# Kernel tuning notes

Hardware: AMD Instinct MI355X
Metric: run time of the kernel (lower is better)

The kernel has to match this reference:

```python
import jax, jax.numpy as jnp
import numpy as np

D_MODEL = 1024
NUM_HEADS = 16
HEAD_DIM = D_MODEL // NUM_HEADS


def setup_inputs() -> dict:
    key = jax.random.key(0)
    ks = jax.random.split(key, 9)
    B, S = 2, 2048
    scale = 1.0 / np.sqrt(D_MODEL)
    inp = {
        "x": jax.random.normal(ks[0], (B, S, D_MODEL), dtype=jnp.float32),
        "Wq": jax.random.normal(ks[1], (D_MODEL, D_MODEL), dtype=jnp.float32) * scale,
        "bq": jnp.zeros((D_MODEL,), dtype=jnp.float32),
        "Wk": jax.random.normal(ks[2], (D_MODEL, D_MODEL), dtype=jnp.float32) * scale,
        "bk": jnp.zeros((D_MODEL,), dtype=jnp.float32),
        "Wv": jax.random.normal(ks[3], (D_MODEL, D_MODEL), dtype=jnp.float32) * scale,
        "bv": jnp.zeros((D_MODEL,), dtype=jnp.float32),
        "Wo": jax.random.normal(ks[4], (D_MODEL, D_MODEL), dtype=jnp.float32) * scale,
        "bo": jnpp_zeros(D_MODEL) if False else jnp.zeros((D_MODEL,), dtype=jnp.float32),
    }
    return inp


def reference(x, Wq, bq, Wk, bk, Wv, bv, Wo, bo):
    B, S, _ = x.shape
    # projections (torch Linear: y = x @ W.T + b; here W stored as [in, out])
    q = x @ Wq + bq  # [B,S,D]
    k = x @ Wk + bk
    v = x @ Wv + bv
    # split heads -> [B,H,S,hd]
    def split(t):
        return t.reshape(B, S, NUM_HEADS, HEAD_DIM).transpose(0, 2, 1, 3)
    q, k, v = split(q), split(k), split(v)
    scale = 1.0 / jnp.sqrt(jnp.asarray(HEAD_DIM, dtype=x.dtype))
    scores = jnp.einsum("bhqd,bhkd->bhqk", q, k) * scale  # [B,H,S,S]
    probs = jax.nn.softmax(scores, axis=-1)
    out = jnp.einsum("bhqk,bhkd->bhqd", probs, v)  # [B,H,S,hd]
    out = out.transpose(0, 2, 1, 3).reshape(B, S, D_MODEL)
    return out @ Wo + bo  # dropout is identity in eval mode
```

## Files before the change

### kernel.cpp

```cpp
#include <hip/hip_runtime.h>

#define D_MODEL 1024
#define NHEADS  16
#define HDIM    64
#define BATCH   2
#define SEQ     2048
#define M_TOK   (BATCH * SEQ)

typedef unsigned short u16;
typedef unsigned int   u32;
typedef __attribute__((ext_vector_type(8))) short  short8;
typedef __attribute__((ext_vector_type(4))) float  floatx4;
typedef __attribute__((ext_vector_type(2))) u32    u32x2;

#define GLOBAL_AS __attribute__((address_space(1)))
#define LDS_AS    __attribute__((address_space(3)))

static __device__ __forceinline__ void gload_lds16(const u16* g, u16* l) {
    __builtin_amdgcn_global_load_lds((const GLOBAL_AS u32*)g, (LDS_AS u32*)l, 16, 0, 0);
}

static __device__ __forceinline__ u16 f2bf(float f) {
    union { float f; u32 i; } v; v.f = f;
    u32 x = v.i;
    return (u16)((x + 0x7fffu + ((x >> 16) & 1u)) >> 16);
}

static __device__ __forceinline__ u32 cvtpk(float a, float b) {
    u32 r;
    asm("v_cvt_pk_bf16_f32 %0, %1, %2" : "=v"(r) : "v"(a), "v"(b));
    return r;
}

static __device__ __forceinline__ short8 ld8_cvt(const float* __restrict__ p) {
    float4 f0 = *(const float4*)(p);
    float4 f1 = *(const float4*)(p + 4);
    short8 r;
    r[0] = (short)f2bf(f0.x); r[1] = (short)f2bf(f0.y);
    r[2] = (short)f2bf(f0.z); r[3] = (short)f2bf(f0.w);
    r[4] = (short)f2bf(f1.x); r[5] = (short)f2bf(f1.y);
    r[6] = (short)f2bf(f1.z); r[7] = (short)f2bf(f1.w);
    return r;
}

__global__ __launch_bounds__(256) void zerofill_k(float* __restrict__ out, int n) {
    int i = blockIdx.x * 256 + threadIdx.x;
    if (i < n) out[i] = 0.f;
}

__global__ __launch_bounds__(256) void prep_k(const float* __restrict__ x,
                                              const float* __restrict__ W0,
                                              const float* __restrict__ W1,
                                              const float* __restrict__ W2,
                                              const float* __restrict__ W3,
                                              u16* __restrict__ WtBase,
                                              u16* __restrict__ Xb) {
    int z = blockIdx.z;
    int t = threadIdx.x;
    if (z == 4) {
        int blk = blockIdx.y * 32 + blockIdx.x;
        size_t i0 = ((size_t)blk * 256 + t) * 16;
        short8 v0 = ld8_cvt(x + i0);
        short8 v1 = ld8_cvt(x + i0 + 8);
        *(short8*)(Xb + i0)     = v0;
        *(short8*)(Xb + i0 + 8) = v1;
        return;
    }
    const float* W = (z == 0) ? W0 : (z == 1) ? W1 : (z == 2) ? W2 : W3;
    u16* Wt = WtBase + (size_t)z * 1024 * 1024;
    __shared__ u16 T[32][34];
    int bx = blockIdx.x * 32, by = blockIdx.y * 32;
    {
        int r = t >> 3, c4 = t & 7;
        float4 f = *(const float4*)(W + (size_t)(by + r) * 1024 + bx + c4 * 4);
        u32 lo = (u32)f2bf(f.x) | ((u32)f2bf(f.y) << 16);
        u32 hi = (u32)f2bf(f.z) | ((u32)f2bf(f.w) << 16);
        *(u32*)(&T[r][c4 * 4])     = lo;
        *(u32*)(&T[r][c4 * 4 + 2]) = hi;
    }
    __syncthreads();
    if (t < 128) {
        int n = t >> 2, seg = t & 3;
        short8 v;
#pragma unroll
        for (int i = 0; i < 8; ++i) v[i] = (short)T[seg * 8 + i][n];
        *(short8*)(Wt + (size_t)(bx + n) * 1024 + by + seg * 8) = v;
    }
}

template <int MODE, int OUTF32, int MI, int BK>
static __device__ __forceinline__ void gemm_core(u16* __restrict__ smem,
                                                 const u16* __restrict__ A,
                                                 const u16* __restrict__ Bt,
                                                 const float* __restrict__ bias,
                                                 float scale,
                                                 void* __restrict__ C,
                                                 int m0, int n0) {
    constexpr int RG   = BK / 8;
    constexpr int BUFG = (MI * 32 + 128) * RG;
    int tid  = threadIdx.x;
    int wave = tid >> 6, lane = tid & 63;
    int quad = lane >> 4, l15 = lane & 15;
    int wm = (wave & 1) * (MI * 16);
    int wn = (wave >> 1) * 64;

    auto stage = [&](int buf, int k0) {
        u16* Asb = smem + (size_t)buf * BUFG * 8;
        u16* Bsb = Asb + MI * 32 * RG * 8;
#pragma unroll
        for (int t = 0; t < MI * 32 * RG / 256; ++t) {
            int a = t * 256 + tid;
            int row = a / RG, c = a & (RG - 1);
            int cs = (BK == 64) ? (c ^ (row & 7)) : c;
            gload_lds16(A + (size_t)(m0 + row) * 1024 + k0 + cs * 8,
                        Asb + (size_t)a * 8);
        }
#pragma unroll
        for (int t = 0; t < 128 * RG / 256; ++t) {
            int a = t * 256 + tid;
            int row = a / RG, c = a & (RG - 1);
            int cs = (BK == 64) ? (c ^ (row & 7)) : c;
            gload_lds16(Bt + (size_t)(n0 + row) * 1024 + k0 + cs * 8,
                        Bsb + (size_t)a * 8);
        }
    };

    floatx4 acc[MI][4] = {};
    stage(0, 0);

    for (int k0 = 0; k0 < 1024; k0 += BK) {
        int cur = (k0 / BK) & 1;
        __syncthreads();
        if (k0 + BK < 1024) stage(cur ^ 1, k0 + BK);

        u16* Asb = smem + (size_t)cur * BUFG * 8;
        u16* Bsb = Asb + MI * 32 * RG * 8;
#pragma unroll
        for (int h = 0; h < BK / 32; ++h) {
            short8 af[MI], bfr[4];
#pragma unroll
            for (int i = 0; i < MI; ++i) {
                int row = wm + i * 16 + l15;
                int g = (BK == 64) ? ((h * 4 + quad) ^ (l15 & 7)) : quad;
                af[i] = *(const short8*)(Asb + (size_t)row * BK + g * 8);
            }
#pragma unroll
            for (int j = 0; j < 4; ++j) {
                int row = wn + j * 16 + l15;
                int g = (BK == 64) ? ((h * 4 + quad) ^ (l15 & 7)) : quad;
                bfr[j] = *(const short8*)(Bsb + (size_t)row * BK + g * 8);
            }
#pragma unroll
            for (int i = 0; i < MI; ++i)
#pragma unroll
                for (int j = 0; j < 4; ++j)
                    acc[i][j] = __builtin_amdgcn_mfma_f32_16x16x32_bf16(af[i], bfr[j], acc[i][j], 0, 0, 0);
        }
    }

    if constexpr (MODE == 2) {
        __syncthreads();
        u16* T = smem;
        int bb = m0 >> 11;
#pragma unroll
        for (int p = 0; p < 2; ++p) {
            if (p) __syncthreads();
            if ((wave >> 1) == p) {
#pragma unroll
                for (int j = 0; j < 4; ++j) {
                    int dcol = j * 16 + l15;
                    float bv = bias[n0 + p * 64 + dcol];
#pragma unroll
                    for (int i = 0; i < MI; ++i) {
#pragma unroll
                        for (int rr = 0; rr < 2; ++rr) {
                            int srow = wm + i * 16 + quad * 4 + rr * 2;
                            u16 lo = f2bf((acc[i][j][rr * 2]     + bv) * scale);
                            u16 hi = f2bf((acc[i][j][rr * 2 + 1] + bv) * scale);
                            *(u32*)(T + dcol * 136 + srow) = (u32)lo | ((u32)hi << 16);
                        }
                    }
                }
            }
            __syncthreads();
            int d  = tid >> 2;
            int sc = (tid & 3) * 32;
            int col = n0 + p * 64 + d;
            int h = col >> 6, dd = col & 63;
            int s0 = (m0 & 2047) + sc;
            size_t gbase = (((size_t)bb * NHEADS + h) * HDIM + dd) * SEQ + s0;
#pragma unroll
            for (int c = 0; c < 4; ++c)
                *(short8*)((u16*)C + gbase + c * 8) = *(const short8*)(T + d * 136 + sc + c * 8);
        }
        return;
    }

#pragma unroll
    for (int j = 0; j < 4; ++j) {
        int col = n0 + wn + j * 16 + l15;
        float bv = bias[col];
#pragma unroll
        for (int i = 0; i < MI; ++i) {
#pragma unroll
            for (int r = 0; r < 4; ++r) {
                int row = m0 + wm + i * 16 + quad * 4 + r;
                float v = (acc[i][j][r] + bv) * scale;
                size_t idx;
                if (MODE == 0) {
                    idx = (size_t)row * 1024 + col;
                } else {
                    int b = row >> 11, s = row & 2047;
                    int h = col >> 6,  d = col & 63;
                    idx = (((size_t)b * NHEADS + h) * SEQ + s) * HDIM + d;
                }
                if constexpr (OUTF32) ((float*)C)[idx] = v;
                else                  ((u16*)C)[idx] = f2bf(v);
            }
        }
    }
}

__global__ __launch_bounds__(256, 3) void gemm_qkv(const u16* __restrict__ X,
                                                   const u16* __restrict__ WtBase,
                                                   const float* __restrict__ bq,
                                                   const float* __restrict__ bk,
                                                   const float* __restrict__ bv,
                                                   u16* __restrict__ OutBase) {
    __shared__ __align__(16) u16 smem[16384];
    int hw  = blockIdx.z * 256 + blockIdx.y * 8 + blockIdx.x;
    int x   = hw & 7;
    int i   = hw >> 3;
    int ml  = i / 24;
    int rem = i - ml * 24;
    int z   = rem >> 3;
    int n0  = (rem & 7) * 128;
    int m0  = (x * 4 + ml) * 128;
    const u16* Bt     = WtBase + (size_t)z * 1024 * 1024;
    const float* bias = (z == 0) ? bq : (z == 1) ? bk : bv;
    u16* C            = OutBase + (size_t)z * (size_t)M_TOK * 1024;
    if (z == 2)
        gemm_core<2, 0, 4, 32>(smem, X, Bt, bias, 1.0f, C, m0, n0);
    else if (z == 0)
        gemm_core<1, 0, 4, 32>(smem, X, Bt, bias, 0.18033688011112042f , C, m0, n0);
    else
        gemm_core<1, 0, 4, 32>(smem, X, Bt, bias, 1.0f, C, m0, n0);
}

__global__ __launch_bounds__(256, 2) void gemm_out(const u16* __restrict__ A,
                                                   const u16* __restrict__ Bt,
                                                   const float* __restrict__ bias,
                                                   float* __restrict__ C) {
    __shared__ __align__(16) u16 smem[24576];
    int hw = blockIdx.y * 8 + blockIdx.x;
    int x  = hw & 7;
    int i  = hw >> 3;
    int m0 = (x * 8 + (i >> 3)) * 64;
    int n0 = (i & 7) * 128;
    gemm_core<0, 1, 2, 64>(smem, A, Bt, bias, 1.0f, C, m0, n0);
}

#define PST2 40
__global__ __launch_bounds__(512, 3) void attn_k(const u16* __restrict__ Q,
                                                 const u16* __restrict__ K,
                                                 const u16* __restrict__ Vt_g,
                                                 u16* __restrict__ O) {
    __shared__ __align__(16) u16 Vt[2][64 * 128];
    __shared__ __align__(16) u16 Kt[2][128 * 64];
    __shared__ __align__(16) u16 Pl[8][16 * PST2];

    int tid  = threadIdx.x;
    int wave = tid >> 6, lane = tid & 63;
    int quad = lane >> 4, l15 = lane & 15;
    int bh = blockIdx.y;
    int b = bh >> 4, h = bh & 15;
    const u16* Qb = Q    + (size_t)bh * SEQ * HDIM;
    const u16* Kb = K    + (size_t)bh * SEQ * HDIM;
    const u16* Vb = Vt_g + (size_t)bh * HDIM * SEQ;
    int q0 = blockIdx.x * 128 + wave * 16;

    short8 qf0 = *(const short8*)(Qb + (size_t)(q0 + l15) * 64 + quad * 8);
    short8 qf1 = *(const short8*)(Qb + (size_t)(q0 + l15) * 64 + 32 + quad * 8);

    short8 onesf;
#pragma unroll
    for (int i = 0; i < 8; ++i) onesf[i] = (short)0x3F80;

    floatx4 o[4] = {};
    floatx4 o_sum = {};

    {
#pragma unroll
        for (int rnd = 0; rnd < 2; ++rnd) {
            int g = rnd * 512 + tid;
            int vrow = g >> 4, vc = g & 15;
            gload_lds16(Vb + (size_t)vrow * SEQ + (vc ^ (vrow & 15)) * 8,
                        Vt[0] + (size_t)g * 8);
            int krow = g >> 3, kc = g & 7;
            gload_lds16(Kb + (size_t)krow * 64 + (kc ^ (krow & 7)) * 8,
                        Kt[0] + (size_t)g * 8);
        }
    }

    for (int it = 0; it < SEQ / 128; ++it) {
        int kv0 = it * 128;
        __syncthreads();

        if (it + 1 < SEQ / 128) {
            u16* vdst = Vt[(it + 1) & 1];
            u16* kdst = Kt[(it + 1) & 1];
#pragma unroll
            for (int rnd = 0; rnd < 2; ++rnd) {
                int g = rnd * 512 + tid;
                int vrow = g >> 4, vc = g & 15;
                gload_lds16(Vb + (size_t)vrow * SEQ + kv0 + 128 + (vc ^ (vrow & 15)) * 8,
                            vdst + (size_t)g * 8);
                int krow = g >> 3, kc = g & 7;
                gload_lds16(Kb + (size_t)(kv0 + 128 + krow) * 64 + (kc ^ (krow & 7)) * 8,
                            kdst + (size_t)g * 8);
            }
        }

        const u16* kb = Kt[it & 1];
        floatx4 s[8];
        __builtin_amdgcn_s_setprio(1);
#pragma unroll
        for (int j = 0; j < 8; ++j) {
            int row = j * 16 + l15;
            const u16* kr = kb + (size_t)row * 64;
            short8 k0 = *(const short8*)(kr + ((quad ^ (l15 & 7)) * 8));
            short8 k1 = *(const short8*)(kr + (((quad + 4) ^ (l15 & 7)) * 8));
            floatx4 a = {};
            a = __builtin_amdgcn_mfma_f32_16x16x32_bf16(k0, qf0, a, 0, 0, 0);
            a = __builtin_amdgcn_mfma_f32_16x16x32_bf16(k1, qf1, a, 0, 0, 0);
            s[j] = a;
        }
        __builtin_amdgcn_s_setprio(0);

        const u16* vb = Vt[it & 1];
#pragma unroll
        for (int kh = 0; kh < 4; ++kh) {
#pragma unroll
            for (int t = 0; t < 2; ++t) {
                int j = kh * 2 + t;
                float p0 = exp2f(s[j][0]), p1 = exp2f(s[j][1]);
                float p2 = exp2f(s[j][2]), p3 = exp2f(s[j][3]);
                u32 w0 = cvtpk(p0, p1), w1 = cvtpk(p2, p3);
                *(u32x2*)(&Pl[wave][l15 * PST2 + t * 16 + quad * 4]) = (u32x2){w0, w1};
            }
            short8 pf = *(const short8*)(&Pl[wave][l15 * PST2 + quad * 8]);
            __builtin_amdgcn_s_setprio(1);
#pragma unroll
            for (int dj = 0; dj < 4; ++dj) {
                int row = dj * 16 + l15;
                int cg  = kh * 4 + quad;
                short8 vf = *(const short8*)(&vb[(row * 16 + (cg ^ l15)) * 8]);
                o[dj] = __builtin_amdgcn_mfma_f32_16x16x32_bf16(pf, vf, o[dj], 0, 0, 0);
            }
            o_sum = __builtin_amdgcn_mfma_f32_16x16x32_bf16(pf, onesf, o_sum, 0, 0, 0);
            __builtin_amdgcn_s_setprio(0);
        }
    }

#pragma unroll
    for (int r = 0; r < 4; ++r) {
        float invq = 1.f / o_sum[r];
        int srow = q0 + quad * 4 + r;
        size_t base = ((size_t)b * SEQ + srow) * D_MODEL + h * HDIM;
#pragma unroll
        for (int dj = 0; dj < 4; ++dj)
            O[base + dj * 16 + l15] = f2bf(o[dj][r] * invq);
    }
}

extern "C" void kernel_launch(void* const* d_in, const int* in_sizes, int n_in,
                              void* d_out, int out_size, void* d_ws, size_t ws_size,
                              hipStream_t stream) {
    const float* x  = (const float*)d_in[0];
    const float* Wq = (const float*)d_in[1];
    const float* bq = (const float*)d_in[2];
    const float* Wk = (const float*)d_in[3];
    const float* bk = (const float*)d_in[4];
    const float* Wv = (const float*)d_in[5];
    const float* bv = (const float*)d_in[6];
    const float* Wo = (const float*)d_in[7];
    const float* bo = (const float*)d_in[8];
    float* out = (float*)d_out;

    char* ws = (char*)d_ws;
    const size_t WSZ = (size_t)1024 * 1024 * sizeof(u16);
    const size_t QSZ = (size_t)M_TOK * 1024 * sizeof(u16);
    const size_t NEED = 4 * WSZ + 4 * QSZ;

    if (ws_size < NEED) {
        zerofill_k<<<dim3((out_size + 255) / 256), 256, 0, stream>>>(out, out_size);
        return;
    }

    u16* wtq = (u16*)(ws);
    u16* wto = (u16*)(ws + 3 * WSZ);
    u16* Qw  = (u16*)(ws + 4 * WSZ);
    u16* Kw  = (u16*)(ws + 4 * WSZ + QSZ);
    u16* Vw  = (u16*)(ws + 4 * WSZ + 2 * QSZ);
    u16* Xb  = (u16*)(ws + 4 * WSZ + 3 * QSZ);
    u16* Aw  = Xb;

    prep_k<<<dim3(32, 32, 5), 256, 0, stream>>>(x, Wq, Wk, Wv, Wo, wtq, Xb);

    gemm_qkv<<<dim3(8, 32, 3), 256, 0, stream>>>(Xb, wtq, bq, bk, bv, Qw);
    attn_k<<<dim3(SEQ / 128, BATCH * NHEADS), 512, 0, stream>>>(Qw, Kw, Vw, Aw);
    gemm_out<<<dim3(8, 64), 256, 0, stream>>>(Aw, wto, bo, out);
}
```

Before: 193.2 us.

## Process two query tiles per wave in attention to reuse K/V fragments

The attention block now uses 4 waves instead of 8, and each wave handles 32 query rows (two 16-row tiles) instead of 16. Every K and V fragment read from LDS feeds two MFMAs, which halves LDS read traffic per unit of compute. The cost is more accumulator and score registers per wave (s doubles to 16 floatx4) and fewer waves per block, which lowers occupancy and the ability to hide latency. Launch bounds drop to 256 threads with 2 blocks per SM.

```diff
diff --git a/kernel.cpp b/kernel.cpp
--- a/kernel.cpp
+++ b/kernel.cpp
@@ -261,13 +261,13 @@
 }
 
 #define PST2 40
-__global__ __launch_bounds__(512, 3) void attn_k(const u16* __restrict__ Q,
+__global__ __launch_bounds__(256, 2) void attn_k(const u16* __restrict__ Q,
                                                  const u16* __restrict__ K,
                                                  const u16* __restrict__ Vt_g,
                                                  u16* __restrict__ O) {
     __shared__ __align__(16) u16 Vt[2][64 * 128];
     __shared__ __align__(16) u16 Kt[2][128 * 64];
-    __shared__ __align__(16) u16 Pl[8][16 * PST2];
+    __shared__ __align__(16) u16 Pl[4][2 * 16 * PST2];
 
     int tid  = threadIdx.x;
     int wave = tid >> 6, lane = tid & 63;
@@ -277,22 +277,27 @@
     const u16* Qb = Q    + (size_t)bh * SEQ * HDIM;
     const u16* Kb = K    + (size_t)bh * SEQ * HDIM;
     const u16* Vb = Vt_g + (size_t)bh * HDIM * SEQ;
-    int q0 = blockIdx.x * 128 + wave * 16;
-
-    short8 qf0 = *(const short8*)(Qb + (size_t)(q0 + l15) * 64 + quad * 8);
-    short8 qf1 = *(const short8*)(Qb + (size_t)(q0 + l15) * 64 + 32 + quad * 8);
+    int q0 = blockIdx.x * 128 + wave * 32;
+
+    short8 qf0[2], qf1[2];
+#pragma unroll
+    for (int qh = 0; qh < 2; ++qh) {
+        const u16* qp = Qb + (size_t)(q0 + qh * 16 + l15) * 64;
+        qf0[qh] = *(const short8*)(qp + quad * 8);
+        qf1[qh] = *(const short8*)(qp + 32 + quad * 8);
+    }
 
     short8 onesf;
 #pragma unroll
     for (int i = 0; i < 8; ++i) onesf[i] = (short)0x3F80;
 
-    floatx4 o[4] = {};
-    floatx4 o_sum = {};
+    floatx4 o[4][2] = {};
+    floatx4 o_sum[2] = {};
 
     {
 #pragma unroll
-        for (int rnd = 0; rnd < 2; ++rnd) {
-            int g = rnd * 512 + tid;
+        for (int rnd = 0; rnd < 4; ++rnd) {
+            int g = rnd * 256 + tid;
             int vrow = g >> 4, vc = g & 15;
             gload_lds16(Vb + (size_t)vrow * SEQ + (vc ^ (vrow & 15)) * 8,
                         Vt[0] + (size_t)g * 8);
@@ -310,8 +315,8 @@
             u16* vdst = Vt[(it + 1) & 1];
             u16* kdst = Kt[(it + 1) & 1];
 #pragma unroll
-            for (int rnd = 0; rnd < 2; ++rnd) {
-                int g = rnd * 512 + tid;
+            for (int rnd = 0; rnd < 4; ++rnd) {
+                int g = rnd * 256 + tid;
                 int vrow = g >> 4, vc = g & 15;
                 gload_lds16(Vb + (size_t)vrow * SEQ + kv0 + 128 + (vc ^ (vrow & 15)) * 8,
                             vdst + (size_t)g * 8);
@@ -322,7 +327,7 @@
         }
 
         const u16* kb = Kt[it & 1];
-        floatx4 s[8];
+        floatx4 s[8][2];
         __builtin_amdgcn_s_setprio(1);
 #pragma unroll
         for (int j = 0; j < 8; ++j) {
@@ -330,10 +335,13 @@
             const u16* kr = kb + (size_t)row * 64;
             short8 k0 = *(const short8*)(kr + ((quad ^ (l15 & 7)) * 8));
             short8 k1 = *(const short8*)(kr + (((quad + 4) ^ (l15 & 7)) * 8));
-            floatx4 a = {};
-            a = __builtin_amdgcn_mfma_f32_16x16x32_bf16(k0, qf0, a, 0, 0, 0);
-            a = __builtin_amdgcn_mfma_f32_16x16x32_bf16(k1, qf1, a, 0, 0, 0);
-            s[j] = a;
+#pragma unroll
+            for (int qh = 0; qh < 2; ++qh) {
+                floatx4 a = {};
+                a = __builtin_amdgcn_mfma_f32_16x16x32_bf16(k0, qf0[qh], a, 0, 0, 0);
+                a = __builtin_amdgcn_mfma_f32_16x16x32_bf16(k1, qf1[qh], a, 0, 0, 0);
+                s[j][qh] = a;
+            }
         }
         __builtin_amdgcn_s_setprio(0);
 
@@ -341,35 +349,49 @@
 #pragma unroll
         for (int kh = 0; kh < 4; ++kh) {
 #pragma unroll
-            for (int t = 0; t < 2; ++t) {
-                int j = kh * 2 + t;
-                float p0 = exp2f(s[j][0]), p1 = exp2f(s[j][1]);
-                float p2 = exp2f(s[j][2]), p3 = exp2f(s[j][3]);
-                u32 w0 = cvtpk(p0, p1), w1 = cvtpk(p2, p3);
-                *(u32x2*)(&Pl[wave][l15 * PST2 + t * 16 + quad * 4]) = (u32x2){w0, w1};
-            }
-            short8 pf = *(const short8*)(&Pl[wave][l15 * PST2 + quad * 8]);
+            for (int qh = 0; qh < 2; ++qh) {
+#pragma unroll
+                for (int t = 0; t < 2; ++t) {
+                    int j = kh * 2 + t;
+                    float p0 = exp2f(s[j][qh][0]), p1 = exp2f(s[j][qh][1]);
+                    float p2 = exp2f(s[j][qh][2]), p3 = exp2f(s[j][qh][3]);
+                    u32 w0 = cvtpk(p0, p1), w1 = cvtpk(p2, p3);
+                    *(u32x2*)(&Pl[wave][qh * 16 * PST2 + l15 * PST2 + t * 16 + quad * 4]) =
+                        (u32x2){w0, w1};
+                }
+            }
+            short8 pf[2];
+#pragma unroll
+            for (int qh = 0; qh < 2; ++qh)
+                pf[qh] = *(const short8*)(&Pl[wave][qh * 16 * PST2 + l15 * PST2 + quad * 8]);
             __builtin_amdgcn_s_setprio(1);
 #pragma unroll
             for (int dj = 0; dj < 4; ++dj) {
                 int row = dj * 16 + l15;
                 int cg  = kh * 4 + quad;
                 short8 vf = *(const short8*)(&vb[(row * 16 + (cg ^ l15)) * 8]);
-                o[dj] = __builtin_amdgcn_mfma_f32_16x16x32_bf16(pf, vf, o[dj], 0, 0, 0);
-            }
-            o_sum = __builtin_amdgcn_mfma_f32_16x16x32_bf16(pf, onesf, o_sum, 0, 0, 0);
+#pragma unroll
+                for (int qh = 0; qh < 2; ++qh)
+                    o[dj][qh] = __builtin_amdgcn_mfma_f32_16x16x32_bf16(pf[qh], vf, o[dj][qh], 0, 0, 0);
+            }
+#pragma unroll
+            for (int qh = 0; qh < 2; ++qh)
+                o_sum[qh] = __builtin_amdgcn_mfma_f32_16x16x32_bf16(pf[qh], onesf, o_sum[qh], 0, 0, 0);
             __builtin_amdgcn_s_setprio(0);
         }
     }
 
 #pragma unroll
-    for (int r = 0; r < 4; ++r) {
-        float invq = 1.f / o_sum[r];
-        int srow = q0 + quad * 4 + r;
-        size_t base = ((size_t)b * SEQ + srow) * D_MODEL + h * HDIM;
-#pragma unroll
-        for (int dj = 0; dj < 4; ++dj)
-            O[base + dj * 16 + l15] = f2bf(o[dj][r] * invq);
+    for (int qh = 0; qh < 2; ++qh) {
+#pragma unroll
+        for (int r = 0; r < 4; ++r) {
+            float invq = 1.f / o_sum[qh][r];
+            int srow = q0 + qh * 16 + quad * 4 + r;
+            size_t base = ((size_t)b * SEQ + srow) * D_MODEL + h * HDIM;
+#pragma unroll
+            for (int dj = 0; dj < 4; ++dj)
+                O[base + dj * 16 + l15] = f2bf(o[dj][qh][r] * invq);
+        }
     }
 }
 
@@ -408,6 +430,6 @@
     prep_k<<<dim3(32, 32, 5), 256, 0, stream>>>(x, Wq, Wk, Wv, Wo, wtq, Xb);
 
     gemm_qkv<<<dim3(8, 32, 3), 256, 0, stream>>>(Xb, wtq, bq, bk, bv, Qw);
-    attn_k<<<dim3(SEQ / 128, BATCH * NHEADS), 512, 0, stream>>>(Qw, Kw, Vw, Aw);
+    attn_k<<<dim3(SEQ / 128, BATCH * NHEADS), 256, 0, stream>>>(Qw, Kw, Vw, Aw);
     gemm_out<<<dim3(8, 64), 256, 0, stream>>>(Aw, wto, bo, out);
 }
```

New measurement: 197.9 us. 2.4% more time.
